# Performance work log

Hardware: AMD Instinct MI355X
Metric: run time of the kernel (lower is better)

## Reference

```python
import jax, jax.numpy as jnp
import numpy as np

B, S, D, N = 8, 4096, 1024, 16
EPS = 1e-6


def setup_inputs() -> dict:
    key = jax.random.key(0)
    ks = jax.random.split(key, 6)
    s = 1.0 / np.sqrt(D)
    return {
        "x": jax.random.normal(ks[0], (B, S, D), dtype=jnp.float32),
        "W_lambda": jax.random.uniform(ks[1], (N, D), jnp.float32, -s, s),
        "b_lambda": jnp.full((N,), 2.0, dtype=jnp.float32),  # nn.init.constant_(bias, 2.0)
        "W_B": jax.random.uniform(ks[2], (N, D), jnp.float32, -s, s),
        "W_C": jax.random.uniform(ks[3], (D, N), jnp.float32, -1.0 / np.sqrt(N), 1.0 / np.sqrt(N)),
        "W_gate": jax.random.uniform(ks[4], (D, D), jnp.float32, -s, s),
        "rms_weight": jnp.ones((D,), dtype=jnp.float32),
    }


def reference(x, W_lambda, b_lambda, W_B, W_C, W_gate, rms_weight):
    # Input-dependent decay and input projection, computed for all timesteps at once
    lam = jax.nn.sigmoid(jnp.einsum("bsd,nd->bsn", x, W_lambda) + b_lambda)  # (B,S,N)
    Bx = jnp.einsum("bsd,nd->bsn", x, W_B)  # (B,S,N)

    def step(h, inp):
        l_t, b_t = inp
        h = l_t * h + b_t  # h_t = lambda_t * h_{t-1} + B_t x_t
        return h, h

    h0 = jnp.zeros((x.shape[0], W_B.shape[0]), dtype=x.dtype)
    _, hs = jax.lax.scan(step, h0, (jnp.swapaxes(lam, 0, 1), jnp.swapaxes(Bx, 0, 1)))
    hs = jnp.swapaxes(hs, 0, 1)  # (B,S,N)

    y = jnp.einsum("bsn,dn->bsd", hs, W_C)  # C @ h_t
    gate = jax.nn.sigmoid(jnp.einsum("bsd,ed->bse", x, W_gate))
    y = gate * y
    # RMSNorm
    rms = jax.lax.rsqrt(jnp.mean(y * y, axis=-1, keepdims=True) + EPS)
    return y * rms * rms_weight
```

## Files before the change

kernel.cpp:

```cpp
#include <hip/hip_runtime.h>

#define DD 1024
#define NN 16
#define SS 4096
#define BBATCH 8
#define TOK (BBATCH*SS)

typedef __attribute__((ext_vector_type(8))) __bf16 bf16x8;
typedef __attribute__((ext_vector_type(4))) __bf16 bf16x4;
typedef __attribute__((ext_vector_type(4))) float f32x4;
typedef unsigned int u32;
typedef unsigned long long u64;

__device__ __forceinline__ void async16(void* lds, const void* g) {
  __builtin_amdgcn_global_load_lds(
      (const __attribute__((address_space(1))) u32*)(u64)(g),
      (__attribute__((address_space(3))) u32*)(u32)(u64)(lds), 16, 0, 0);
}

__device__ __forceinline__ float sigmoidf_(float v) {
  return 1.f / (1.f + __expf(-v));
}

__global__ __launch_bounds__(256)
void k_proj(const float* __restrict__ x, const float* __restrict__ wlf,
            const float* __restrict__ wbf, const float* __restrict__ b_lambda,
            __bf16* __restrict__ xb, float* __restrict__ lam, float* __restrict__ bx) {
  __shared__ __align__(16) __bf16 sA[64 * 32];
  __shared__ __align__(16) __bf16 sB[32 * 32];
  int tid = threadIdx.x;
  int lane = tid & 63, w = tid >> 6;
  int tok0 = blockIdx.x * 64;
  int r15 = lane & 15, kg = lane >> 4;
  int crow = tid >> 2, cg = tid & 3;
  const float* xsrc = x + (u64)(tok0 + crow) * DD + cg * 8;
  __bf16* xdst = xb + (u64)(tok0 + crow) * DD + cg * 8;
  u32 aoff = (u32)crow * 64 + ((u32)(cg ^ (crow & 3) ^ ((crow >> 2) & 3)) << 4);
  const float* wsrc = nullptr;
  u32 boff = 0;
  if (tid < 128) {
    int wrow = tid >> 2, wcg = tid & 3;
    wsrc = (wrow < 16 ? wlf + (u64)wrow * DD : wbf + (u64)(wrow - 16) * DD) + wcg * 8;
    boff = (u32)wrow * 64 + ((u32)(wcg ^ (wrow & 3)) << 4);
  }
  int arow = w * 16 + r15;
  u32 aro = (u32)arow * 64 + ((u32)(kg ^ (arow & 3) ^ ((arow >> 2) & 3)) << 4);
  u32 bro0 = (u32)r15 * 64 + ((u32)(kg ^ (r15 & 3)) << 4);
  int brow1 = 16 + r15;
  u32 bro1 = (u32)brow1 * 64 + ((u32)(kg ^ (brow1 & 3)) << 4);
  f32x4 acc0 = {}, acc1 = {};
  float4 cx0 = *(const float4*)(xsrc);
  float4 cx1 = *(const float4*)(xsrc + 4);
  float4 cw0 = {}, cw1 = {};
  if (tid < 128) { cw0 = *(const float4*)(wsrc); cw1 = *(const float4*)(wsrc + 4); }
  for (int kt = 0; kt < 32; ++kt) {
    float4 nx0, nx1, nw0 = {}, nw1 = {};
    if (kt < 31) {
      nx0 = *(const float4*)(xsrc + (kt + 1) * 32);
      nx1 = *(const float4*)(xsrc + (kt + 1) * 32 + 4);
      if (tid < 128) {
        nw0 = *(const float4*)(wsrc + (kt + 1) * 32);
        nw1 = *(const float4*)(wsrc + (kt + 1) * 32 + 4);
      }
    }
    bf16x8 cv;
    cv[0] = (__bf16)cx0.x; cv[1] = (__bf16)cx0.y; cv[2] = (__bf16)cx0.z; cv[3] = (__bf16)cx0.w;
    cv[4] = (__bf16)cx1.x; cv[5] = (__bf16)cx1.y; cv[6] = (__bf16)cx1.z; cv[7] = (__bf16)cx1.w;
    *(bf16x8*)(xdst + kt * 32) = cv;
    *(bf16x8*)((char*)sA + aoff) = cv;
    if (tid < 128) {
      bf16x8 wv;
      wv[0] = (__bf16)cw0.x; wv[1] = (__bf16)cw0.y; wv[2] = (__bf16)cw0.z; wv[3] = (__bf16)cw0.w;
      wv[4] = (__bf16)cw1.x; wv[5] = (__bf16)cw1.y; wv[6] = (__bf16)cw1.z; wv[7] = (__bf16)cw1.w;
      *(bf16x8*)((char*)sB + boff) = wv;
    }
    __syncthreads();
    bf16x8 af = *(const bf16x8*)((const char*)sA + aro);
    bf16x8 b0 = *(const bf16x8*)((const char*)sB + bro0);
    bf16x8 b1 = *(const bf16x8*)((const char*)sB + bro1);
    acc0 = __builtin_amdgcn_mfma_f32_16x16x32_bf16(af, b0, acc0, 0, 0, 0);
    acc1 = __builtin_amdgcn_mfma_f32_16x16x32_bf16(af, b1, acc1, 0, 0, 0);
    __syncthreads();
    if (kt < 31) { cx0 = nx0; cx1 = nx1; cw0 = nw0; cw1 = nw1; }
  }
  float bl = b_lambda[r15];
#pragma unroll
  for (int r = 0; r < 4; ++r) {
    int token = tok0 + w * 16 + kg * 4 + r;
    lam[token * NN + r15] = sigmoidf_(acc0[r] + bl);
    bx[token * NN + r15] = acc1[r];
  }
}

__global__ __launch_bounds__(256)
void k_scan(const float* __restrict__ lam, const float* __restrict__ bx,
            float* __restrict__ hs, const float* __restrict__ wgf,
            __bf16* __restrict__ wg) {
  if (blockIdx.x >= BBATCH * NN) {
    int i = (blockIdx.x - BBATCH * NN) * 256 + threadIdx.x;
    const float* src = wgf + (u64)i * 8;
    float4 a = *(const float4*)src, b = *(const float4*)(src + 4);
    bf16x8 o;
    o[0] = (__bf16)a.x; o[1] = (__bf16)a.y; o[2] = (__bf16)a.z; o[3] = (__bf16)a.w;
    o[4] = (__bf16)b.x; o[5] = (__bf16)b.y; o[6] = (__bf16)b.z; o[7] = (__bf16)b.w;
    *(bf16x8*)(wg + (u64)i * 8) = o;
    return;
  }
  int b = blockIdx.x >> 4, n = blockIdx.x & 15;
  int t = threadIdx.x;
  const int CH = SS / 256;
  float lv[CH], bv[CH];
  int base = (b * SS + t * CH) * NN + n;
  float a = 1.f, bacc = 0.f;
#pragma unroll
  for (int i = 0; i < CH; ++i) {
    lv[i] = lam[base + i * NN];
    bv[i] = bx[base + i * NN];
    bacc = lv[i] * bacc + bv[i];
    a *= lv[i];
  }
  __shared__ float As[2][256], Bs[2][256];
  As[0][t] = a; Bs[0][t] = bacc;
  __syncthreads();
  int cur = 0;
  for (int off = 1; off < 256; off <<= 1) {
    float a2 = As[cur][t], b2 = Bs[cur][t];
    if (t >= off) {
      float ap = As[cur][t - off], bp = Bs[cur][t - off];
      b2 = b2 + a2 * bp;
      a2 = a2 * ap;
    }
    As[cur ^ 1][t] = a2; Bs[cur ^ 1][t] = b2;
    cur ^= 1;
    __syncthreads();
  }
  float h = (t == 0) ? 0.f : Bs[cur][t - 1];
#pragma unroll
  for (int i = 0; i < CH; ++i) {
    h = lv[i] * h + bv[i];
    hs[base + i * NN] = h;
  }
}

#define STAGE(tile, M, h) do {                                                    \
    u32 lds0 = (u32)(((((tile) & 1) * 4 + (M) * 2 + (h)) << 14) + tid * 16);      \
    u64 g0 = ((M) ? bBase : aBase) + ((u64)(h) << 18) + (u64)(tile) * 128;        \
    async16(smc + lds0, (const void*)g0);                                         \
    async16(smc + lds0 + 8192, (const void*)(g0 + 131072));                       \
  } while (0)

template<int YB16>
__global__ __launch_bounds__(512, 2)
void k_gemm(const __bf16* __restrict__ xb, const __bf16* __restrict__ wg,
            const float* __restrict__ hs, const float* __restrict__ wc,
            float* __restrict__ outf, __bf16* __restrict__ outb) {
  __shared__ __align__(16) char smc[131072];
  const int tid = threadIdx.x, lane = tid & 63, w = tid >> 6;
  const int r15 = lane & 15, kg = lane >> 4;
  const int wr = w >> 2, wcq = w & 3;
  int bid = blockIdx.x;
  int swz = (bid & 7) * 64 + (bid >> 3);
  int m = swz >> 2, n = swz & 3;
  const int tok0 = m * 256, n0 = n * 256;
  const int sslot = (tid & 7) ^ ((tid >> 3) & 7);
  const u64 aBase = (u64)(const char*)xb + (u64)(tok0 + (tid >> 3)) * 2048 + (u32)sslot * 16;
  const u64 bBase = (u64)(const char*)wg + (u64)(n0 + (tid >> 3)) * 2048 + (u32)sslot * 16;
  const u32 sxa0 = (u32)(((0 | kg) ^ (r15 & 7)) * 16);
  const u32 sxa1 = (u32)(((4 | kg) ^ (r15 & 7)) * 16);
  const u32 lrB0 = (u32)((wcq & 1) * 64);

  f32x4 acc[8][4] = {};

  STAGE(0, 0, 0); STAGE(0, 0, 1); STAGE(0, 1, 0); STAGE(0, 1, 1);
  STAGE(1, 1, 0); STAGE(1, 1, 1); STAGE(1, 0, 0);
  asm volatile("s_waitcnt vmcnt(6)" ::: "memory");
  __builtin_amdgcn_s_barrier();
  asm volatile("" ::: "memory");

  for (int k = 0; k < 16; ++k) {
    const int b = k & 1;
    const char* Ah = smc + (u32)((b * 4 + wr) << 14);
    const char* Bh = smc + (u32)((b * 4 + 2 + (wcq >> 1)) << 14);
    bf16x8 af[8][2], bfr[4][2];
#pragma unroll
    for (int mt = 0; mt < 2; ++mt) {
      u32 ro = (u32)(mt * 16 + r15) * 128;
      af[mt][0] = *(const bf16x8*)(Ah + ro + sxa0);
      af[mt][1] = *(const bf16x8*)(Ah + ro + sxa1);
    }
#pragma unroll
    for (int nt = 0; nt < 4; ++nt) {
      u32 ro = (lrB0 + (u32)(nt * 16 + r15)) * 128;
      bfr[nt][0] = *(const bf16x8*)(Bh + ro + sxa0);
      bfr[nt][1] = *(const bf16x8*)(Bh + ro + sxa1);
    }
    if (k <= 14) STAGE(k + 1, 0, 1);
    __builtin_amdgcn_s_barrier();
    __builtin_amdgcn_s_setprio(1);
#pragma unroll
    for (int mt = 0; mt < 2; ++mt)
#pragma unroll
      for (int nt = 0; nt < 4; ++nt) {
        acc[mt][nt] = __builtin_amdgcn_mfma_f32_16x16x32_bf16(af[mt][0], bfr[nt][0], acc[mt][nt], 0, 0, 0);
        acc[mt][nt] = __builtin_amdgcn_mfma_f32_16x16x32_bf16(af[mt][1], bfr[nt][1], acc[mt][nt], 0, 0, 0);
      }
    __builtin_amdgcn_s_setprio(0);
    __builtin_amdgcn_s_barrier();
    asm volatile("" ::: "memory");
#pragma unroll
    for (int mt = 2; mt < 6; ++mt) {
      u32 ro = (u32)(mt * 16 + r15) * 128;
      af[mt][0] = *(const bf16x8*)(Ah + ro + sxa0);
      af[mt][1] = *(const bf16x8*)(Ah + ro + sxa1);
    }
    if (k <= 13) STAGE(k + 2, 1, 0);
    __builtin_amdgcn_s_barrier();
    __builtin_amdgcn_s_setprio(1);
#pragma unroll
    for (int mt = 2; mt < 4; ++mt)
#pragma unroll
      for (int nt = 0; nt < 4; ++nt) {
        acc[mt][nt] = __builtin_amdgcn_mfma_f32_16x16x32_bf16(af[mt][0], bfr[nt][0], acc[mt][nt], 0, 0, 0);
        acc[mt][nt] = __builtin_amdgcn_mfma_f32_16x16x32_bf16(af[mt][1], bfr[nt][1], acc[mt][nt], 0, 0, 0);
      }
    __builtin_amdgcn_s_setprio(0);
    __builtin_amdgcn_s_barrier();
    asm volatile("" ::: "memory");
#pragma unroll
    for (int mt = 6; mt < 8; ++mt) {
      u32 ro = (u32)(mt * 16 + r15) * 128;
      af[mt][0] = *(const bf16x8*)(Ah + ro + sxa0);
      af[mt][1] = *(const bf16x8*)(Ah + ro + sxa1);
    }
    if (k <= 13) STAGE(k + 2, 1, 1);
    __builtin_amdgcn_s_barrier();
    __builtin_amdgcn_s_setprio(1);
#pragma unroll
    for (int mt = 4; mt < 6; ++mt)
#pragma unroll
      for (int nt = 0; nt < 4; ++nt) {
        acc[mt][nt] = __builtin_amdgcn_mfma_f32_16x16x32_bf16(af[mt][0], bfr[nt][0], acc[mt][nt], 0, 0, 0);
        acc[mt][nt] = __builtin_amdgcn_mfma_f32_16x16x32_bf16(af[mt][1], bfr[nt][1], acc[mt][nt], 0, 0, 0);
      }
    __builtin_amdgcn_s_setprio(0);
    __builtin_amdgcn_s_barrier();
    asm volatile("" ::: "memory");
    if (k <= 13) STAGE(k + 2, 0, 0);
    if (k <= 13)      asm volatile("s_waitcnt vmcnt(6)" ::: "memory");
    else if (k == 14) asm volatile("s_waitcnt vmcnt(0)" ::: "memory");
    __builtin_amdgcn_s_barrier();
    asm volatile("" ::: "memory");
    __builtin_amdgcn_s_setprio(1);
#pragma unroll
    for (int mt = 6; mt < 8; ++mt)
#pragma unroll
      for (int nt = 0; nt < 4; ++nt) {
        acc[mt][nt] = __builtin_amdgcn_mfma_f32_16x16x32_bf16(af[mt][0], bfr[nt][0], acc[mt][nt], 0, 0, 0);
        acc[mt][nt] = __builtin_amdgcn_mfma_f32_16x16x32_bf16(af[mt][1], bfr[nt][1], acc[mt][nt], 0, 0, 0);
      }
    __builtin_amdgcn_s_setprio(0);
  }
  asm volatile("" ::: "memory");

  __bf16* hsH = (__bf16*)smc;
  __bf16* hsL = (__bf16*)(smc + 16384);
  __bf16* wcB = (__bf16*)(smc + 32768);
  {
    int row = tid >> 1, half = tid & 1;
    const float* hp = hs + (u64)(tok0 + row) * NN + half * 8;
    const float* wp2 = wc + (u64)(n0 + row) * NN + half * 8;
    float4 h0 = *(const float4*)hp, h1 = *(const float4*)(hp + 4);
    float4 w0 = *(const float4*)wp2, w1 = *(const float4*)(wp2 + 4);
    bf16x8 hh, hl, wb, zz = {};
    float hv[8] = {h0.x, h0.y, h0.z, h0.w, h1.x, h1.y, h1.z, h1.w};
    float wv[8] = {w0.x, w0.y, w0.z, w0.w, w1.x, w1.y, w1.z, w1.w};
#pragma unroll
    for (int e = 0; e < 8; ++e) {
      __bf16 hi = (__bf16)hv[e];
      hh[e] = hi;
      hl[e] = (__bf16)(hv[e] - (float)hi);
      wb[e] = (__bf16)wv[e];
    }
    u32 realOff = (u32)row * 32 + (u32)((half ^ (row & 3)) << 3);
    u32 zeroOff = (u32)row * 32 + (u32)(((2 + half) ^ (row & 3)) << 3);
    *(bf16x8*)(hsH + realOff) = hh;  *(bf16x8*)(hsH + zeroOff) = zz;
    *(bf16x8*)(hsL + realOff) = hl;  *(bf16x8*)(hsL + zeroOff) = zz;
    *(bf16x8*)(wcB + realOff) = wb;  *(bf16x8*)(wcB + zeroOff) = zz;
  }
  __syncthreads();
  bf16x8 bw[4];
#pragma unroll
  for (int nt = 0; nt < 4; ++nt) {
    int row = wcq * 64 + nt * 16 + r15;
    bw[nt] = *(const bf16x8*)(wcB + row * 32 + ((kg ^ (row & 3)) << 3));
  }
  const f32x4 zero4 = {};
#pragma unroll
  for (int mt = 0; mt < 8; ++mt) {
    int arow = wr * 128 + mt * 16 + r15;
    u32 ao = (u32)arow * 32 + (u32)((kg ^ (arow & 3)) << 3);
    bf16x8 ah = *(const bf16x8*)(hsH + ao);
    bf16x8 al = *(const bf16x8*)(hsL + ao);
#pragma unroll
    for (int nt = 0; nt < 4; ++nt) {
      f32x4 cy4 = __builtin_amdgcn_mfma_f32_16x16x32_bf16(al, bw[nt], zero4, 0, 0, 0);
      cy4 = __builtin_amdgcn_mfma_f32_16x16x32_bf16(ah, bw[nt], cy4, 0, 0, 0);
      int j = wcq * 64 + nt * 16 + r15;
#pragma unroll
      for (int r = 0; r < 4; ++r) {
        int i = wr * 128 + mt * 16 + kg * 4 + r;
        float g = sigmoidf_(acc[mt][nt][r]);
        u64 off = (u64)(tok0 + i) * DD + n0 + j;
        if (YB16) outb[off] = (__bf16)(g * cy4[r]);
        else      outf[off] = g * cy4[r];
      }
    }
  }
}

__global__ __launch_bounds__(256)
void k_norm_b(const __bf16* __restrict__ yb, float* __restrict__ out,
              const float* __restrict__ rw) {
  int row = blockIdx.x * 4 + (threadIdx.x >> 6);
  int lane = threadIdx.x & 63;
  const __bf16* yrow = yb + (u64)row * DD;
  bf16x4 v[4];
  float f[16];
  float rs = 0.f;
#pragma unroll
  for (int q = 0; q < 4; ++q) {
    v[q] = *(const bf16x4*)(yrow + q * 256 + lane * 4);
#pragma unroll
    for (int e = 0; e < 4; ++e) {
      f[q * 4 + e] = (float)v[q][e];
      rs += f[q * 4 + e] * f[q * 4 + e];
    }
  }
#pragma unroll
  for (int msk = 1; msk < 64; msk <<= 1) rs += __shfl_xor(rs, msk, 64);
  float rstd = rsqrtf(rs * (1.f / DD) + 1e-6f);
  float* orow = out + (u64)row * DD;
#pragma unroll
  for (int q = 0; q < 4; ++q) {
    float4 wv = *(const float4*)(rw + q * 256 + lane * 4);
    float4 o;
    o.x = f[q * 4 + 0] * rstd * wv.x;
    o.y = f[q * 4 + 1] * rstd * wv.y;
    o.z = f[q * 4 + 2] * rstd * wv.z;
    o.w = f[q * 4 + 3] * rstd * wv.w;
    *(float4*)(orow + q * 256 + lane * 4) = o;
  }
}

__global__ __launch_bounds__(256)
void k_norm_f(float* __restrict__ out, const float* __restrict__ rw) {
  int row = blockIdx.x * 4 + (threadIdx.x >> 6);
  int lane = threadIdx.x & 63;
  float4* p = (float4*)(out + (u64)row * DD);
  float4 v[4];
  float rs = 0.f;
#pragma unroll
  for (int e = 0; e < 4; ++e) {
    v[e] = p[e * 64 + lane];
    rs += v[e].x * v[e].x + v[e].y * v[e].y + v[e].z * v[e].z + v[e].w * v[e].w;
  }
#pragma unroll
  for (int msk = 1; msk < 64; msk <<= 1) rs += __shfl_xor(rs, msk, 64);
  float rstd = rsqrtf(rs * (1.f / DD) + 1e-6f);
  const float4* rwp = (const float4*)rw;
#pragma unroll
  for (int e = 0; e < 4; ++e) {
    float4 wv = rwp[e * 64 + lane];
    float4 o;
    o.x = v[e].x * rstd * wv.x;
    o.y = v[e].y * rstd * wv.y;
    o.z = v[e].z * rstd * wv.z;
    o.w = v[e].w * rstd * wv.w;
    p[e * 64 + lane] = o;
  }
}

extern "C" void kernel_launch(void* const* d_in, const int* in_sizes, int n_in,
                              void* d_out, int out_size, void* d_ws, size_t ws_size,
                              hipStream_t stream) {
  (void)in_sizes; (void)n_in; (void)out_size;
  const float* x        = (const float*)d_in[0];
  const float* W_lambda = (const float*)d_in[1];
  const float* b_lambda = (const float*)d_in[2];
  const float* W_B      = (const float*)d_in[3];
  const float* W_C      = (const float*)d_in[4];
  const float* W_gate   = (const float*)d_in[5];
  const float* rms_w    = (const float*)d_in[6];
  char* ws = (char*)d_ws;
  __bf16* xb  = (__bf16*)(ws + 0);
  __bf16* wg  = (__bf16*)(ws + 67108864);
  float*  lam = (float*)(ws + 69271552);
  float*  bx  = (float*)(ws + 71368704);
  float*  hs  = (float*)(ws + 73465856);
  __bf16* yb  = (__bf16*)(ws + 75563008);
  float*  out = (float*)d_out;
  bool yb16 = ws_size >= (size_t)(75563008ull + 67108864ull);

  k_proj<<<TOK / 64, 256, 0, stream>>>(x, W_lambda, W_B, b_lambda, xb, lam, bx);
  k_scan<<<BBATCH * NN + DD * DD / 8 / 256, 256, 0, stream>>>(lam, bx, hs, W_gate, wg);
  if (yb16) {
    k_gemm<1><<<(TOK / 256) * (DD / 256), 512, 0, stream>>>(xb, wg, hs, W_C, nullptr, yb);
    k_norm_b<<<TOK / 4, 256, 0, stream>>>(yb, out, rms_w);
  } else {
    k_gemm<0><<<(TOK / 256) * (DD / 256), 512, 0, stream>>>(xb, wg, hs, W_C, out, nullptr);
    k_norm_f<<<TOK / 4, 256, 0, stream>>>(out, rms_w);
  }
}
```

Measured before the change: 183.3 us.

## Software-pipeline LDS fragment reads one phase ahead of MFMA clusters in gate GEMM

Restructures the GEMM main loop so each phase's LDS fragment reads happen one phase earlier. The A/B fragments for the next k-step's first cluster are read at the end of the current iteration, and each later cluster's A rows are read before the preceding MFMA cluster runs. Fragment storage is split into separate register arrays, with sched_barriers to hold the ordering. The aim is to hide LDS read latency behind MFMA work, at the cost of more live registers and a subtler barrier and async-load ordering that could race with buffer reuse.

Measured after the change: 182.6 us. Within noise of the previous version (-0.4%).

```diff
diff --git a/kernel.cpp b/kernel.cpp
--- a/kernel.cpp
+++ b/kernel.cpp
@@ -149,6 +149,23 @@
     async16(smc + lds0 + 8192, (const void*)(g0 + 131072));                       \
   } while (0)
 
+#define READ12(bb) do {                                                           \
+    const char* Ah_ = smc + (u32)(((bb) * 4 + wr) << 14);                         \
+    const char* Bh_ = smc + (u32)(((bb) * 4 + 2 + (wcq >> 1)) << 14);             \
+    _Pragma("unroll")                                                             \
+    for (int mt = 0; mt < 2; ++mt) {                                              \
+      u32 ro = (u32)(mt * 16 + r15) * 128;                                        \
+      af01[mt][0] = *(const bf16x8*)(Ah_ + ro + sxa0);                            \
+      af01[mt][1] = *(const bf16x8*)(Ah_ + ro + sxa1);                            \
+    }                                                                             \
+    _Pragma("unroll")                                                             \
+    for (int nt = 0; nt < 4; ++nt) {                                              \
+      u32 ro = (lrB0 + (u32)(nt * 16 + r15)) * 128;                               \
+      bfr[nt][0] = *(const bf16x8*)(Bh_ + ro + sxa0);                             \
+      bfr[nt][1] = *(const bf16x8*)(Bh_ + ro + sxa1);                             \
+    }                                                                             \
+  } while (0)
+
 template<int YB16>
 __global__ __launch_bounds__(512, 2)
 void k_gemm(const __bf16* __restrict__ xb, const __bf16* __restrict__ wg,
@@ -170,58 +187,35 @@
   const u32 lrB0 = (u32)((wcq & 1) * 64);
 
   f32x4 acc[8][4] = {};
+  bf16x8 af01[2][2], af25[4][2], af67[2][2], bfr[4][2];
 
   STAGE(0, 0, 0); STAGE(0, 0, 1); STAGE(0, 1, 0); STAGE(0, 1, 1);
   STAGE(1, 1, 0); STAGE(1, 1, 1); STAGE(1, 0, 0);
   asm volatile("s_waitcnt vmcnt(6)" ::: "memory");
   __builtin_amdgcn_s_barrier();
   asm volatile("" ::: "memory");
+  READ12(0);
+  __builtin_amdgcn_sched_barrier(0);
 
   for (int k = 0; k < 16; ++k) {
     const int b = k & 1;
     const char* Ah = smc + (u32)((b * 4 + wr) << 14);
-    const char* Bh = smc + (u32)((b * 4 + 2 + (wcq >> 1)) << 14);
-    bf16x8 af[8][2], bfr[4][2];
-#pragma unroll
-    for (int mt = 0; mt < 2; ++mt) {
-      u32 ro = (u32)(mt * 16 + r15) * 128;
-      af[mt][0] = *(const bf16x8*)(Ah + ro + sxa0);
-      af[mt][1] = *(const bf16x8*)(Ah + ro + sxa1);
-    }
-#pragma unroll
-    for (int nt = 0; nt < 4; ++nt) {
-      u32 ro = (lrB0 + (u32)(nt * 16 + r15)) * 128;
-      bfr[nt][0] = *(const bf16x8*)(Bh + ro + sxa0);
-      bfr[nt][1] = *(const bf16x8*)(Bh + ro + sxa1);
-    }
-    if (k <= 14) STAGE(k + 1, 0, 1);
-    __builtin_amdgcn_s_barrier();
-    __builtin_amdgcn_s_setprio(1);
-#pragma unroll
-    for (int mt = 0; mt < 2; ++mt)
-#pragma unroll
-      for (int nt = 0; nt < 4; ++nt) {
-        acc[mt][nt] = __builtin_amdgcn_mfma_f32_16x16x32_bf16(af[mt][0], bfr[nt][0], acc[mt][nt], 0, 0, 0);
-        acc[mt][nt] = __builtin_amdgcn_mfma_f32_16x16x32_bf16(af[mt][1], bfr[nt][1], acc[mt][nt], 0, 0, 0);
-      }
-    __builtin_amdgcn_s_setprio(0);
-    __builtin_amdgcn_s_barrier();
-    asm volatile("" ::: "memory");
 #pragma unroll
     for (int mt = 2; mt < 6; ++mt) {
       u32 ro = (u32)(mt * 16 + r15) * 128;
-      af[mt][0] = *(const bf16x8*)(Ah + ro + sxa0);
-      af[mt][1] = *(const bf16x8*)(Ah + ro + sxa1);
-    }
-    if (k <= 13) STAGE(k + 2, 1, 0);
+      af25[mt - 2][0] = *(const bf16x8*)(Ah + ro + sxa0);
+      af25[mt - 2][1] = *(const bf16x8*)(Ah + ro + sxa1);
+    }
+    __builtin_amdgcn_sched_barrier(0);
+    if (k <= 14) STAGE(k + 1, 0, 1);
     __builtin_amdgcn_s_barrier();
     __builtin_amdgcn_s_setprio(1);
 #pragma unroll
-    for (int mt = 2; mt < 4; ++mt)
+    for (int mt = 0; mt < 2; ++mt)
 #pragma unroll
       for (int nt = 0; nt < 4; ++nt) {
-        acc[mt][nt] = __builtin_amdgcn_mfma_f32_16x16x32_bf16(af[mt][0], bfr[nt][0], acc[mt][nt], 0, 0, 0);
-        acc[mt][nt] = __builtin_amdgcn_mfma_f32_16x16x32_bf16(af[mt][1], bfr[nt][1], acc[mt][nt], 0, 0, 0);
+        acc[mt][nt] = __builtin_amdgcn_mfma_f32_16x16x32_bf16(af01[mt][0], bfr[nt][0], acc[mt][nt], 0, 0, 0);
+        acc[mt][nt] = __builtin_amdgcn_mfma_f32_16x16x32_bf16(af01[mt][1], bfr[nt][1], acc[mt][nt], 0, 0, 0);
       }
     __builtin_amdgcn_s_setprio(0);
     __builtin_amdgcn_s_barrier();
@@ -229,9 +223,23 @@
 #pragma unroll
     for (int mt = 6; mt < 8; ++mt) {
       u32 ro = (u32)(mt * 16 + r15) * 128;
-      af[mt][0] = *(const bf16x8*)(Ah + ro + sxa0);
-      af[mt][1] = *(const bf16x8*)(Ah + ro + sxa1);
-    }
+      af67[mt - 6][0] = *(const bf16x8*)(Ah + ro + sxa0);
+      af67[mt - 6][1] = *(const bf16x8*)(Ah + ro + sxa1);
+    }
+    __builtin_amdgcn_sched_barrier(0);
+    if (k <= 13) STAGE(k + 2, 1, 0);
+    __builtin_amdgcn_s_barrier();
+    __builtin_amdgcn_s_setprio(1);
+#pragma unroll
+    for (int mt = 2; mt < 4; ++mt)
+#pragma unroll
+      for (int nt = 0; nt < 4; ++nt) {
+        acc[mt][nt] = __builtin_amdgcn_mfma_f32_16x16x32_bf16(af25[mt - 2][0], bfr[nt][0], acc[mt][nt], 0, 0, 0);
+        acc[mt][nt] = __builtin_amdgcn_mfma_f32_16x16x32_bf16(af25[mt - 2][1], bfr[nt][1], acc[mt][nt], 0, 0, 0);
+      }
+    __builtin_amdgcn_s_setprio(0);
+    __builtin_amdgcn_s_barrier();
+    asm volatile("" ::: "memory");
     if (k <= 13) STAGE(k + 2, 1, 1);
     __builtin_amdgcn_s_barrier();
     __builtin_amdgcn_s_setprio(1);
@@ -239,8 +247,8 @@
     for (int mt = 4; mt < 6; ++mt)
 #pragma unroll
       for (int nt = 0; nt < 4; ++nt) {
-        acc[mt][nt] = __builtin_amdgcn_mfma_f32_16x16x32_bf16(af[mt][0], bfr[nt][0], acc[mt][nt], 0, 0, 0);
-        acc[mt][nt] = __builtin_amdgcn_mfma_f32_16x16x32_bf16(af[mt][1], bfr[nt][1], acc[mt][nt], 0, 0, 0);
+        acc[mt][nt] = __builtin_amdgcn_mfma_f32_16x16x32_bf16(af25[mt - 2][0], bfr[nt][0], acc[mt][nt], 0, 0, 0);
+        acc[mt][nt] = __builtin_amdgcn_mfma_f32_16x16x32_bf16(af25[mt - 2][1], bfr[nt][1], acc[mt][nt], 0, 0, 0);
       }
     __builtin_amdgcn_s_setprio(0);
     __builtin_amdgcn_s_barrier();
@@ -255,12 +263,17 @@
     for (int mt = 6; mt < 8; ++mt)
 #pragma unroll
       for (int nt = 0; nt < 4; ++nt) {
-        acc[mt][nt] = __builtin_amdgcn_mfma_f32_16x16x32_bf16(af[mt][0], bfr[nt][0], acc[mt][nt], 0, 0, 0);
-        acc[mt][nt] = __builtin_amdgcn_mfma_f32_16x16x32_bf16(af[mt][1], bfr[nt][1], acc[mt][nt], 0, 0, 0);
+        acc[mt][nt] = __builtin_amdgcn_mfma_f32_16x16x32_bf16(af67[mt - 6][0], bfr[nt][0], acc[mt][nt], 0, 0, 0);
+        acc[mt][nt] = __builtin_amdgcn_mfma_f32_16x16x32_bf16(af67[mt - 6][1], bfr[nt][1], acc[mt][nt], 0, 0, 0);
       }
     __builtin_amdgcn_s_setprio(0);
+    if (k < 15) {
+      READ12(b ^ 1);
+      __builtin_amdgcn_sched_barrier(0);
+    }
   }
   asm volatile("" ::: "memory");
+  __builtin_amdgcn_s_barrier();
 
   __bf16* hsH = (__bf16*)smc;
   __bf16* hsL = (__bf16*)(smc + 16384);
```
